# Optimization experiments

Measured on AMD Instinct MI355X. Metric: run time of the kernel, lower is better.

The kernel has to match this reference:

```python
import jax, jax.numpy as jnp
import numpy as np

B, L, S, DIM, H, DH, DFF = 2, 2048, 2048, 1024, 16, 64, 4096
EPS = 1e-6


def _ln(x, w, b):
    m = jnp.mean(x, axis=-1, keepdims=True)
    v = jnp.mean(jnp.square(x - m), axis=-1, keepdims=True)
    return (x - m) / jnp.sqrt(v + EPS) * w + b


def _mha(q, k, v, mask):
    # q: [B,L,H*DH], k/v: [B,S,H*DH], mask broadcastable to [B,H,L,S], True = masked
    b, l, _ = q.shape
    s = k.shape[1]
    q = q.reshape(b, l, H, DH)
    k = k.reshape(b, s, H, DH)
    v = v.reshape(b, s, H, DH)
    scale = 1.0 / np.sqrt(DH).astype(np.float32)
    attn = jnp.einsum('blhd,bshd->bhls', q, k) * scale
    if mask is not None:
        attn = jnp.where(mask, -jnp.inf, attn)
    attn = jax.nn.softmax(attn, axis=-1)
    out = jnp.einsum('bhls,bshd->blhd', attn, v)
    return out.reshape(b, l, H * DH)


def setup_inputs() -> dict:
    key = jax.random.key(0)
    ks = jax.random.split(key, 12)
    std = 0.02
    inp = {
        'input': jax.random.normal(ks[0], (B, L, DIM), jnp.float32),
        'source': jax.random.normal(ks[1], (B, S, DIM), jnp.float32),
        # source mask: no source positions masked
        'source_mask': jnp.zeros((B, 1, 1, S), bool),
        # causal mask for self-attention (True above diagonal -> masked)
        'mask': jnp.triu(jnp.ones((L, L), bool), 1)[None, None],
        # self-attention
        'ln_self_w': jnp.ones((DIM,), jnp.float32),
        'ln_self_b': jnp.zeros((DIM,), jnp.float32),
        'w_qkv': std * jax.random.normal(ks[2], (DIM, 3 * DIM), jnp.float32),
        'b_qkv': jnp.zeros((3 * DIM,), jnp.float32),
        'w_so': std * jax.random.normal(ks[3], (DIM, DIM), jnp.float32),
        'b_so': jnp.zeros((DIM,), jnp.float32),
        # cross-attention
        'ln_cross_w': jnp.ones((DIM,), jnp.float32),
        'ln_cross_b': jnp.zeros((DIM,), jnp.float32),
        'w_q': std * jax.random.normal(ks[4], (DIM, DIM), jnp.float32),
        'b_q': jnp.zeros((DIM,), jnp.float32),
        'w_kv': std * jax.random.normal(ks[5], (DIM, 2 * DIM), jnp.float32),
        'b_kv': jnp.zeros((2 * DIM,), jnp.float32),
        'w_co': std * jax.random.normal(ks[6], (DIM, DIM), jnp.float32),
        'b_co': jnp.zeros((DIM,), jnp.float32),
        # MLP (1 layer)
        'ln_mlp_w': jnp.ones((DIM,), jnp.float32),
        'ln_mlp_b': jnp.zeros((DIM,), jnp.float32),
        'w_ff1': std * jax.random.normal(ks[7], (DIM, DFF), jnp.float32),
        'b_ff1': jnp.zeros((DFF,), jnp.float32),
        'w_ff2': std * jax.random.normal(ks[8], (DFF, DIM), jnp.float32),
        'b_ff2': jnp.zeros((DIM,), jnp.float32),
    }
    return inp


def reference(input, source, source_mask, mask,
              ln_self_w, ln_self_b, w_qkv, b_qkv, w_so, b_so,
              ln_cross_w, ln_cross_b, w_q, b_q, w_kv, b_kv, w_co, b_co,
              ln_mlp_w, ln_mlp_b, w_ff1, b_ff1, w_ff2, b_ff2):
    x = input
    # self-attention block (pre-LN)
    h = _ln(x, ln_self_w, ln_self_b)
    qkv = h @ w_qkv + b_qkv
    q, k, v = jnp.split(qkv, 3, axis=-1)
    sa = _mha(q, k, v, mask) @ w_so + b_so
    x = x + sa
    # cross-attention block (pre-LN)
    h = _ln(x, ln_cross_w, ln_cross_b)
    q = h @ w_q + b_q
    kv = source @ w_kv + b_kv
    k, v = jnp.split(kv, 2, axis=-1)
    ca = _mha(q, k, v, source_mask) @ w_co + b_co
    x = x + ca
    # feed-forward block (pre-LN), eval mode (no dropout/droppath)
    h = _ln(x, ln_mlp_w, ln_mlp_b)
    ff = jax.nn.gelu(h @ w_ff1 + b_ff1, approximate=False) @ w_ff2 + b_ff2
    x = x + ff
    return x
```

## Files before the change

kernel.cpp:

```cpp
#include <hip/hip_runtime.h>
#include <hip/hip_bf16.h>
#include <math.h>

typedef __bf16 bf16_t;
typedef __bf16 bf16x8 __attribute__((ext_vector_type(8)));
typedef __bf16 bf16x4 __attribute__((ext_vector_type(4)));
typedef float  f32x4  __attribute__((ext_vector_type(4)));

#define DIM   1024
#define NB    2
#define NL    2048
#define NS    2048
#define NH    16
#define NDH   64
#define NDFF  4096

#define DS_READ_B128(dst, addr) \
    asm volatile("ds_read_b128 %0, %1" : "=v"(dst) : "v"(addr))
#define LGKM0_FENCE() do { \
    asm volatile("s_waitcnt lgkmcnt(0)" ::: "memory"); \
    __builtin_amdgcn_sched_barrier(0); } while (0)

__device__ __forceinline__ bf16x8 ld_bf16x8(const bf16_t* p) {
    return *reinterpret_cast<const bf16x8*>(p);
}

__device__ __forceinline__ void gl_lds16(const bf16_t* g, bf16_t* l) {
    __builtin_amdgcn_global_load_lds(
        (const __attribute__((address_space(1))) void*)g,
        (__attribute__((address_space(3))) void*)l, 16, 0, 0);
}

__device__ __forceinline__ unsigned lds_u32(const bf16_t* p) {
    return (unsigned)(uintptr_t)(__attribute__((address_space(3))) const void*)p;
}

__global__ __launch_bounds__(256)
void wconv_kernel(const float* __restrict__ in, bf16_t* __restrict__ out, int K, int N)
{
    __shared__ float tile[32][33];
    int n0 = blockIdx.x * 32, k0 = blockIdx.y * 32;
    int tx = threadIdx.x & 31, ty = threadIdx.x >> 5;
    #pragma unroll
    for (int j = 0; j < 4; ++j)
        tile[ty + 8*j][tx] = in[(size_t)(k0 + ty + 8*j) * N + n0 + tx];
    __syncthreads();
    #pragma unroll
    for (int j = 0; j < 4; ++j)
        out[(size_t)(n0 + ty + 8*j) * K + k0 + tx] = (bf16_t)tile[tx][ty + 8*j];
}

__global__ __launch_bounds__(256)
void f2b_kernel(const float* __restrict__ in, bf16_t* __restrict__ out)
{
    size_t i = ((size_t)blockIdx.x * 256 + threadIdx.x) * 4;
    float4 v = *reinterpret_cast<const float4*>(in + i);
    bf16x4 o = { (bf16_t)v.x, (bf16_t)v.y, (bf16_t)v.z, (bf16_t)v.w };
    *reinterpret_cast<bf16x4*>(out + i) = o;
}

__global__ __launch_bounds__(256)
void ln_kernel(const float* __restrict__ x, const float* __restrict__ wgt,
               const float* __restrict__ bia, bf16_t* __restrict__ out)
{
    int row = blockIdx.x, tid = threadIdx.x;
    float4 xv = reinterpret_cast<const float4*>(x + (size_t)row * DIM)[tid];
    float s1 = xv.x + xv.y + xv.z + xv.w;
    float s2 = xv.x*xv.x + xv.y*xv.y + xv.z*xv.z + xv.w*xv.w;
    #pragma unroll
    for (int off = 32; off > 0; off >>= 1) {
        s1 += __shfl_xor(s1, off, 64);
        s2 += __shfl_xor(s2, off, 64);
    }
    __shared__ float red[8];
    int w = tid >> 6;
    if ((tid & 63) == 0) { red[w] = s1; red[w + 4] = s2; }
    __syncthreads();
    s1 = red[0] + red[1] + red[2] + red[3];
    s2 = red[4] + red[5] + red[6] + red[7];
    float mean = s1 * (1.0f / DIM);
    float var  = s2 * (1.0f / DIM) - mean * mean;
    float rstd = rsqrtf(var + 1e-6f);
    float4 wv = reinterpret_cast<const float4*>(wgt)[tid];
    float4 bv = reinterpret_cast<const float4*>(bia)[tid];
    bf16x4 o = { (bf16_t)((xv.x - mean) * rstd * wv.x + bv.x),
                 (bf16_t)((xv.y - mean) * rstd * wv.y + bv.y),
                 (bf16_t)((xv.z - mean) * rstd * wv.z + bv.z),
                 (bf16_t)((xv.w - mean) * rstd * wv.w + bv.w) };
    reinterpret_cast<bf16x4*>(out + (size_t)row * DIM)[tid] = o;
}

template<int EPI, int BM, int BN>
__global__ __launch_bounds__(512)
void gemm_kernel(const bf16_t* __restrict__ A, const bf16_t* __restrict__ BT,
                 const float* __restrict__ bias, const float* __restrict__ res,
                 void* __restrict__ out, int M, int N, int K)
{
    constexpr int WM = BM / 2, WN = BN / 4;
    constexpr int AM = WM / 16, AN = WN / 16;
    constexpr int ABE = (BM + BN) * 64;
    __shared__ __align__(16) bf16_t lds[2 * ABE];

    int tid = threadIdx.x;
    int lane = tid & 63, w = tid >> 6;
    int wr = w >> 2, wc = w & 3;
    int la = lane & 15, lg = lane >> 4;

    int gx = gridDim.x;
    int flat = blockIdx.y * gx + blockIdx.x;
    int cpx = gx >> 3;
    int xcd = flat & 7, loc = flat >> 3;
    int m0 = (loc / cpx) * BM;
    int n0 = (xcd * cpx + loc % cpx) * BN;

    f32x4 acc[AM][AN] = {};

    int srl  = lane >> 3;
    int sch  = lane & 7;
    int scol = ((sch ^ srl) * 8);
    const bf16_t* Ap = A  + (size_t)(m0 + w * 8 + srl) * K + scol;
    const bf16_t* Bp = BT + (size_t)(n0 + w * 8 + srl) * K + scol;

    auto stage = [&](int t, int buf) {
        int k0 = t * 64;
        bf16_t* base = &lds[buf * ABE];
        #pragma unroll
        for (int i = 0; i < BM / 64; ++i)
            gl_lds16(Ap + ((size_t)i * 64) * K + k0, base + (i * 64 + w * 8) * 64);
        #pragma unroll
        for (int i = 0; i < BN / 64; ++i)
            gl_lds16(Bp + ((size_t)i * 64) * K + k0, base + (BM + i * 64 + w * 8) * 64);
    };

    unsigned ldsb = lds_u32(lds);
    unsigned kla = la & 7;
    unsigned a_base = ldsb + (wr * WM + la) * 128 + ((lg ^ kla) * 16);
    unsigned b_base = ldsb + BM * 128 + (wc * WN + la) * 128 + ((lg ^ kla) * 16);

    auto compute = [&](int buf) {
        unsigned dB = (unsigned)(buf * ABE * 2);
        bf16x8 af[AM], bfr[AN];
        #pragma unroll
        for (int mi = 0; mi < AM; ++mi)
            DS_READ_B128(af[mi], a_base + dB + mi * 2048);
        #pragma unroll
        for (int ni = 0; ni < AN; ++ni)
            DS_READ_B128(bfr[ni], b_base + dB + ni * 2048);
        LGKM0_FENCE();
        __builtin_amdgcn_s_setprio(1);
        #pragma unroll
        for (int mi = 0; mi < AM; ++mi)
            #pragma unroll
            for (int ni = 0; ni < AN; ++ni)
                acc[mi][ni] = __builtin_amdgcn_mfma_f32_16x16x32_bf16(
                                  af[mi], bfr[ni], acc[mi][ni], 0, 0, 0);
        __builtin_amdgcn_s_setprio(0);
        #pragma unroll
        for (int mi = 0; mi < AM; ++mi)
            DS_READ_B128(af[mi], (a_base + dB + mi * 2048) ^ 64u);
        #pragma unroll
        for (int ni = 0; ni < AN; ++ni)
            DS_READ_B128(bfr[ni], (b_base + dB + ni * 2048) ^ 64u);
        LGKM0_FENCE();
        __builtin_amdgcn_s_setprio(1);
        #pragma unroll
        for (int mi = 0; mi < AM; ++mi)
            #pragma unroll
            for (int ni = 0; ni < AN; ++ni)
                acc[mi][ni] = __builtin_amdgcn_mfma_f32_16x16x32_bf16(
                                  af[mi], bfr[ni], acc[mi][ni], 0, 0, 0);
        __builtin_amdgcn_s_setprio(0);
    };

    int nt = K / 64;
    stage(0, 0);
    for (int t = 0; t < nt; ++t) {
        asm volatile("s_waitcnt vmcnt(0)" ::: "memory");
        __builtin_amdgcn_s_barrier();
        __builtin_amdgcn_sched_barrier(0);
        if (t + 1 < nt) stage(t + 1, (t + 1) & 1);
        compute(t & 1);
    }

    #pragma unroll
    for (int mi = 0; mi < AM; ++mi) {
        #pragma unroll
        for (int ni = 0; ni < AN; ++ni) {
            #pragma unroll
            for (int i = 0; i < 4; ++i) {
                int row = m0 + wr * WM + mi * 16 + lg * 4 + i;
                int col = n0 + wc * WN + ni * 16 + la;
                float v = acc[mi][ni][i] + bias[col];
                if (EPI == 1) v = 0.5f * v * (1.0f + erff(v * 0.70710678118f));
                if (EPI == 2)
                    ((float*)out)[(size_t)row * N + col] = res[(size_t)row * N + col] + v;
                else
                    ((bf16_t*)out)[(size_t)row * N + col] = (bf16_t)v;
            }
        }
    }
}

template<bool CAUSAL>
__global__ __launch_bounds__(512)
void attn_kernel(const bf16_t* __restrict__ Q, int qs,
                 const bf16_t* __restrict__ Kp, int ks,
                 const bf16_t* __restrict__ Vp, int vs,
                 bf16_t* __restrict__ O, int os, int L, int S)
{
    __shared__ __align__(16) bf16_t Ks[64 * 64];
    __shared__ __align__(16) bf16_t Vt[64 * 64];
    __shared__ __align__(16) bf16_t Ps[8][16 * 64];

    int tid = threadIdx.x, lane = tid & 63, w = tid >> 6;
    int la = lane & 15, lg = lane >> 4;
    int qtile = (CAUSAL ? (gridDim.x - 1 - blockIdx.x) : blockIdx.x) * 128;
    int b = blockIdx.y >> 4, h = blockIdx.y & 15;

    const bf16_t* qb = Q  + (size_t)(b * L) * qs + h * 64;
    const bf16_t* kb = Kp + (size_t)(b * S) * ks + h * 64;
    const bf16_t* vb = Vp + (size_t)(b * S) * vs + h * 64;
    bf16_t*       ob = O  + (size_t)(b * L) * os + h * 64;

    int qrow = qtile + w * 16 + la;
    bf16x8 qf0 = ld_bf16x8(qb + (size_t)qrow * qs + lg * 8);
    bf16x8 qf1 = ld_bf16x8(qb + (size_t)qrow * qs + 32 + lg * 8);
    #pragma unroll
    for (int j = 0; j < 8; ++j) {
        qf0[j] = qf0[j] * (bf16_t)0.125f;
        qf1[j] = qf1[j] * (bf16_t)0.125f;
    }

    f32x4 zero = {0.f, 0.f, 0.f, 0.f};
    f32x4 o[4];
    #pragma unroll
    for (int dt = 0; dt < 4; ++dt) o[dt] = zero;
    float lpart[4] = {0.f, 0.f, 0.f, 0.f};

    int rk    = tid >> 3;
    int ck8   = tid & 7;
    int sv    = tid & 63;
    int dbase = (tid >> 6) * 8;
    int r7 = la & 7;

    int n_full = (CAUSAL ? qtile : S) / 64;
    int nit = n_full + (CAUSAL ? 2 : 0);

    bf16x8 kr = ld_bf16x8(kb + (size_t)rk * ks + ck8 * 8);
    bf16x8 vr = ld_bf16x8(vb + (size_t)sv * vs + dbase);

    for (int it = 0; it < nit; ++it) {
        int s0 = it * 64;
        bool diag = CAUSAL && (it >= n_full);

        __syncthreads();
        *reinterpret_cast<bf16x8*>(&Ks[rk * 64 + ((ck8 ^ (rk & 7)) * 8)]) = kr;
        #pragma unroll
        for (int j = 0; j < 8; ++j)
            Vt[(dbase + j) * 64 + (sv ^ (j << 3))] = vr[j];
        __syncthreads();

        if (it + 1 < nit) {
            int s1 = s0 + 64;
            kr = ld_bf16x8(kb + (size_t)(s1 + rk) * ks + ck8 * 8);
            vr = ld_bf16x8(vb + (size_t)(s1 + sv) * vs + dbase);
        }

        f32x4 sf[4];
        #pragma unroll
        for (int ct = 0; ct < 4; ++ct) {
            const bf16_t* kp = &Ks[(ct * 16 + la) * 64];
            bf16x8 k0 = ld_bf16x8(kp + ((lg ^ r7) * 8));
            bf16x8 k1 = ld_bf16x8(kp + (((4 + lg) ^ r7) * 8));
            f32x4 z = zero;
            __builtin_amdgcn_s_setprio(1);
            z = __builtin_amdgcn_mfma_f32_16x16x32_bf16(qf0, k0, z, 0, 0, 0);
            z = __builtin_amdgcn_mfma_f32_16x16x32_bf16(qf1, k1, z, 0, 0, 0);
            __builtin_amdgcn_s_setprio(0);
            sf[ct] = z;
        }

        #pragma unroll
        for (int ct = 0; ct < 4; ++ct) {
            #pragma unroll
            for (int i = 0; i < 4; ++i) {
                float p = __expf(sf[ct][i]);
                if (diag) {
                    int sg = s0 + ct * 16 + la;
                    int qg = qtile + w * 16 + lg * 4 + i;
                    if (sg > qg) p = 0.f;
                }
                lpart[i] += p;
                int row = lg * 4 + i;
                Ps[w][row * 64 + ((ct * 16 + la) ^ ((row & 7) << 3))] = (bf16_t)p;
            }
        }

        bf16x8 pa0 = ld_bf16x8(&Ps[w][la * 64 + ((lg ^ r7) * 8)]);
        bf16x8 pa1 = ld_bf16x8(&Ps[w][la * 64 + (((4 + lg) ^ r7) * 8)]);
        __builtin_amdgcn_s_setprio(1);
        #pragma unroll
        for (int dt = 0; dt < 4; ++dt) {
            const bf16_t* vp = &Vt[(dt * 16 + la) * 64];
            bf16x8 v0 = ld_bf16x8(vp + ((lg ^ r7) * 8));
            bf16x8 v1 = ld_bf16x8(vp + (((4 + lg) ^ r7) * 8));
            o[dt] = __builtin_amdgcn_mfma_f32_16x16x32_bf16(pa0, v0, o[dt], 0, 0, 0);
            o[dt] = __builtin_amdgcn_mfma_f32_16x16x32_bf16(pa1, v1, o[dt], 0, 0, 0);
        }
        __builtin_amdgcn_s_setprio(0);
    }

    #pragma unroll
    for (int off = 1; off < 16; off <<= 1)
        #pragma unroll
        for (int i = 0; i < 4; ++i)
            lpart[i] += __shfl_xor(lpart[i], off, 64);

    #pragma unroll
    for (int dt = 0; dt < 4; ++dt)
        #pragma unroll
        for (int i = 0; i < 4; ++i) {
            int row = qtile + w * 16 + lg * 4 + i;
            float val = o[dt][i] / lpart[i];
            ob[(size_t)row * os + dt * 16 + la] = (bf16_t)val;
        }
}

extern "C" void kernel_launch(void* const* d_in, const int* in_sizes, int n_in,
                              void* d_out, int out_size, void* d_ws, size_t ws_size,
                              hipStream_t stream)
{
    const float* input     = (const float*)d_in[0];
    const float* source    = (const float*)d_in[1];
    const float* ln_self_w = (const float*)d_in[4];
    const float* ln_self_b = (const float*)d_in[5];
    const float* w_qkv     = (const float*)d_in[6];
    const float* b_qkv     = (const float*)d_in[7];
    const float* w_so      = (const float*)d_in[8];
    const float* b_so      = (const float*)d_in[9];
    const float* ln_cross_w= (const float*)d_in[10];
    const float* ln_cross_b= (const float*)d_in[11];
    const float* w_q       = (const float*)d_in[12];
    const float* b_q       = (const float*)d_in[13];
    const float* w_kv      = (const float*)d_in[14];
    const float* b_kv      = (const float*)d_in[15];
    const float* w_co      = (const float*)d_in[16];
    const float* b_co      = (const float*)d_in[17];
    const float* ln_mlp_w  = (const float*)d_in[18];
    const float* ln_mlp_b  = (const float*)d_in[19];
    const float* w_ff1     = (const float*)d_in[20];
    const float* b_ff1     = (const float*)d_in[21];
    const float* w_ff2     = (const float*)d_in[22];
    const float* b_ff2     = (const float*)d_in[23];

    const int M = NB * NL;

    char* ws = (char*)d_ws;
    size_t off = 0;
    auto alloc = [&](size_t bytes) { char* p = ws + off; off += (bytes + 255) & ~(size_t)255; return p; };

    bf16_t* wT_qkv = (bf16_t*)alloc((size_t)3072 * 1024 * 2);
    bf16_t* wT_so  = (bf16_t*)alloc((size_t)1024 * 1024 * 2);
    bf16_t* wT_q   = (bf16_t*)alloc((size_t)1024 * 1024 * 2);
    bf16_t* wT_kv  = (bf16_t*)alloc((size_t)2048 * 1024 * 2);
    bf16_t* wT_co  = (bf16_t*)alloc((size_t)1024 * 1024 * 2);
    bf16_t* wT_ff1 = (bf16_t*)alloc((size_t)4096 * 1024 * 2);
    bf16_t* wT_ff2 = (bf16_t*)alloc((size_t)1024 * 4096 * 2);
    bf16_t* srcb   = (bf16_t*)alloc((size_t)M * 1024 * 2);
    bf16_t* hbuf   = (bf16_t*)alloc((size_t)M * 1024 * 2);
    bf16_t* qkvb   = (bf16_t*)alloc((size_t)M * 3072 * 2);
    bf16_t* attnb  = (bf16_t*)alloc((size_t)M * 1024 * 2);
    bf16_t* qcb    = (bf16_t*)alloc((size_t)M * 1024 * 2);
    bf16_t* kvcb   = (bf16_t*)alloc((size_t)M * 2048 * 2);
    float*  xbuf   = (float*) alloc((size_t)M * 1024 * 4);
    bf16_t* ff1b   = (bf16_t*)alloc((size_t)M * 4096 * 2);
    (void)ws_size; (void)n_in; (void)in_sizes; (void)out_size;

    wconv_kernel<<<dim3(3072/32, 1024/32), 256, 0, stream>>>(w_qkv, wT_qkv, 1024, 3072);
    wconv_kernel<<<dim3(1024/32, 1024/32), 256, 0, stream>>>(w_so,  wT_so,  1024, 1024);
    wconv_kernel<<<dim3(1024/32, 1024/32), 256, 0, stream>>>(w_q,   wT_q,   1024, 1024);
    wconv_kernel<<<dim3(2048/32, 1024/32), 256, 0, stream>>>(w_kv,  wT_kv,  1024, 2048);
    wconv_kernel<<<dim3(1024/32, 1024/32), 256, 0, stream>>>(w_co,  wT_co,  1024, 1024);
    wconv_kernel<<<dim3(4096/32, 1024/32), 256, 0, stream>>>(w_ff1, wT_ff1, 1024, 4096);
    wconv_kernel<<<dim3(1024/32, 4096/32), 256, 0, stream>>>(w_ff2, wT_ff2, 4096, 1024);
    f2b_kernel<<<(M * 1024) / (256 * 4), 256, 0, stream>>>(source, srcb);

    ln_kernel<<<M, 256, 0, stream>>>(input, ln_self_w, ln_self_b, hbuf);
    gemm_kernel<0,128,128><<<dim3(3072/128, M/128), 512, 0, stream>>>(hbuf, wT_qkv, b_qkv, nullptr, qkvb, M, 3072, 1024);
    attn_kernel<true><<<dim3(NL/128, NB*NH), 512, 0, stream>>>(qkvb, 3072, qkvb + 1024, 3072, qkvb + 2048, 3072,
                                                               attnb, 1024, NL, NL);
    gemm_kernel<2,128,64><<<dim3(1024/64, M/128), 512, 0, stream>>>(attnb, wT_so, b_so, input, xbuf, M, 1024, 1024);

    ln_kernel<<<M, 256, 0, stream>>>(xbuf, ln_cross_w, ln_cross_b, hbuf);
    gemm_kernel<0,128,64><<<dim3(1024/64, M/128), 512, 0, stream>>>(hbuf, wT_q, b_q, nullptr, qcb, M, 1024, 1024);
    gemm_kernel<0,128,128><<<dim3(2048/128, M/128), 512, 0, stream>>>(srcb, wT_kv, b_kv, nullptr, kvcb, M, 2048, 1024);
    attn_kernel<false><<<dim3(NL/128, NB*NH), 512, 0, stream>>>(qcb, 1024, kvcb, 2048, kvcb + 1024, 2048,
                                                                attnb, 1024, NL, NS);
    gemm_kernel<2,128,64><<<dim3(1024/64, M/128), 512, 0, stream>>>(attnb, wT_co, b_co, xbuf, xbuf, M, 1024, 1024);

    ln_kernel<<<M, 256, 0, stream>>>(xbuf, ln_mlp_w, ln_mlp_b, hbuf);
    gemm_kernel<1,128,128><<<dim3(4096/128, M/128), 512, 0, stream>>>(hbuf, wT_ff1, b_ff1, nullptr, ff1b, M, 4096, 1024);
    gemm_kernel<2,128,64><<<dim3(1024/64, M/128), 512, 0, stream>>>(ff1b, wT_ff2, b_ff2, xbuf, d_out, M, 1024, 4096);
}
```

Measured before the change: 387.5 us.

## Split attention KV range across two blocks and combine partial outputs

Both attention launches gain a third grid dimension of two splits, each covering half of the key/value tiles. Each split writes unnormalized fp32 output and row sums to scratch buffers that reuse ff1b, qcb and hbuf. A new elementwise kernel adds the two partials, divides by the combined sum and writes bf16. The goal is to double the number of blocks and even out causal work across CUs. The cost is an extra launch plus a large fp32 round trip through global memory per attention.

```diff
diff --git a/kernel.cpp b/kernel.cpp
--- a/kernel.cpp
+++ b/kernel.cpp
@@ -206,7 +206,8 @@
 void attn_kernel(const bf16_t* __restrict__ Q, int qs,
                  const bf16_t* __restrict__ Kp, int ks,
                  const bf16_t* __restrict__ Vp, int vs,
-                 bf16_t* __restrict__ O, int os, int L, int S)
+                 float* __restrict__ o_part, float* __restrict__ l_part,
+                 int L, int S)
 {
     __shared__ __align__(16) bf16_t Ks[64 * 64];
     __shared__ __align__(16) bf16_t Vt[64 * 64];
@@ -216,11 +217,11 @@
     int la = lane & 15, lg = lane >> 4;
     int qtile = (CAUSAL ? (gridDim.x - 1 - blockIdx.x) : blockIdx.x) * 128;
     int b = blockIdx.y >> 4, h = blockIdx.y & 15;
+    int split = blockIdx.z;
 
     const bf16_t* qb = Q  + (size_t)(b * L) * qs + h * 64;
     const bf16_t* kb = Kp + (size_t)(b * S) * ks + h * 64;
     const bf16_t* vb = Vp + (size_t)(b * S) * vs + h * 64;
-    bf16_t*       ob = O  + (size_t)(b * L) * os + h * 64;
 
     int qrow = qtile + w * 16 + la;
     bf16x8 qf0 = ld_bf16x8(qb + (size_t)qrow * qs + lg * 8);
@@ -244,12 +245,15 @@
     int r7 = la & 7;
 
     int n_full = (CAUSAL ? qtile : S) / 64;
-    int nit = n_full + (CAUSAL ? 2 : 0);
-
-    bf16x8 kr = ld_bf16x8(kb + (size_t)rk * ks + ck8 * 8);
-    bf16x8 vr = ld_bf16x8(vb + (size_t)sv * vs + dbase);
-
-    for (int it = 0; it < nit; ++it) {
+    int ntot = CAUSAL ? (n_full + 2) : (S / 64);
+    int mid = ntot >> 1;
+    int lo = split ? mid : 0;
+    int hi = split ? ntot : mid;
+
+    bf16x8 kr = ld_bf16x8(kb + (size_t)(lo * 64 + rk) * ks + ck8 * 8);
+    bf16x8 vr = ld_bf16x8(vb + (size_t)(lo * 64 + sv) * vs + dbase);
+
+    for (int it = lo; it < hi; ++it) {
         int s0 = it * 64;
         bool diag = CAUSAL && (it >= n_full);
 
@@ -260,7 +264,7 @@
             Vt[(dbase + j) * 64 + (sv ^ (j << 3))] = vr[j];
         __syncthreads();
 
-        if (it + 1 < nit) {
+        if (it + 1 < hi) {
             int s1 = s0 + 64;
             kr = ld_bf16x8(kb + (size_t)(s1 + rk) * ks + ck8 * 8);
             vr = ld_bf16x8(vb + (size_t)(s1 + sv) * vs + dbase);
@@ -317,13 +321,31 @@
             lpart[i] += __shfl_xor(lpart[i], off, 64);
 
     #pragma unroll
-    for (int dt = 0; dt < 4; ++dt)
-        #pragma unroll
-        for (int i = 0; i < 4; ++i) {
-            int row = qtile + w * 16 + lg * 4 + i;
-            float val = o[dt][i] / lpart[i];
-            ob[(size_t)row * os + dt * 16 + la] = (bf16_t)val;
-        }
+    for (int i = 0; i < 4; ++i) {
+        size_t rowg = (size_t)(b * L + qtile + w * 16 + lg * 4 + i);
+        #pragma unroll
+        for (int dt = 0; dt < 4; ++dt)
+            o_part[((size_t)split * 4096 + rowg) * 1024 + h * 64 + dt * 16 + la] = o[dt][i];
+        if (la == 0)
+            l_part[((size_t)split * 4096 + rowg) * 16 + h] = lpart[i];
+    }
+}
+
+__global__ __launch_bounds__(256)
+void attn_comb_kernel(const float* __restrict__ op, const float* __restrict__ lp,
+                      bf16_t* __restrict__ out)
+{
+    size_t i = ((size_t)blockIdx.x * 256 + threadIdx.x) * 4;
+    const size_t OS = (size_t)4096 * 1024;
+    float4 a = *reinterpret_cast<const float4*>(op + i);
+    float4 c = *reinterpret_cast<const float4*>(op + OS + i);
+    size_t row = i >> 10;
+    int h = (int)((i & 1023) >> 6);
+    float l = lp[row * 16 + h] + lp[(4096 + row) * 16 + h];
+    float rl = 1.0f / l;
+    bf16x4 o = { (bf16_t)((a.x + c.x) * rl), (bf16_t)((a.y + c.y) * rl),
+                 (bf16_t)((a.z + c.z) * rl), (bf16_t)((a.w + c.w) * rl) };
+    *reinterpret_cast<bf16x4*>(out + i) = o;
 }
 
 extern "C" void kernel_launch(void* const* d_in, const int* in_sizes, int n_in,
@@ -376,6 +398,8 @@
     bf16_t* ff1b   = (bf16_t*)alloc((size_t)M * 4096 * 2);
     (void)ws_size; (void)n_in; (void)in_sizes; (void)out_size;
 
+    float* o_part = (float*)ff1b;
+
     wconv_kernel<<<dim3(3072/32, 1024/32), 256, 0, stream>>>(w_qkv, wT_qkv, 1024, 3072);
     wconv_kernel<<<dim3(1024/32, 1024/32), 256, 0, stream>>>(w_so,  wT_so,  1024, 1024);
     wconv_kernel<<<dim3(1024/32, 1024/32), 256, 0, stream>>>(w_q,   wT_q,   1024, 1024);
@@ -387,15 +411,17 @@
 
     ln_kernel<<<M, 256, 0, stream>>>(input, ln_self_w, ln_self_b, hbuf);
     gemm_kernel<0,128,128><<<dim3(3072/128, M/128), 512, 0, stream>>>(hbuf, wT_qkv, b_qkv, nullptr, qkvb, M, 3072, 1024);
-    attn_kernel<true><<<dim3(NL/128, NB*NH), 512, 0, stream>>>(qkvb, 3072, qkvb + 1024, 3072, qkvb + 2048, 3072,
-                                                               attnb, 1024, NL, NL);
+    attn_kernel<true><<<dim3(NL/128, NB*NH, 2), 512, 0, stream>>>(qkvb, 3072, qkvb + 1024, 3072, qkvb + 2048, 3072,
+                                                                  o_part, (float*)qcb, NL, NL);
+    attn_comb_kernel<<<(M * 1024) / (256 * 4), 256, 0, stream>>>(o_part, (float*)qcb, attnb);
     gemm_kernel<2,128,64><<<dim3(1024/64, M/128), 512, 0, stream>>>(attnb, wT_so, b_so, input, xbuf, M, 1024, 1024);
 
     ln_kernel<<<M, 256, 0, stream>>>(xbuf, ln_cross_w, ln_cross_b, hbuf);
     gemm_kernel<0,128,64><<<dim3(1024/64, M/128), 512, 0, stream>>>(hbuf, wT_q, b_q, nullptr, qcb, M, 1024, 1024);
     gemm_kernel<0,128,128><<<dim3(2048/128, M/128), 512, 0, stream>>>(srcb, wT_kv, b_kv, nullptr, kvcb, M, 2048, 1024);
-    attn_kernel<false><<<dim3(NL/128, NB*NH), 512, 0, stream>>>(qcb, 1024, kvcb, 2048, kvcb + 1024, 2048,
-                                                                attnb, 1024, NL, NS);
+    attn_kernel<false><<<dim3(NL/128, NB*NH, 2), 512, 0, stream>>>(qcb, 1024, kvcb, 2048, kvcb + 1024, 2048,
+                                                                   o_part, (float*)hbuf, NL, NS);
+    attn_comb_kernel<<<(M * 1024) / (256 * 4), 256, 0, stream>>>(o_part, (float*)hbuf, attnb);
     gemm_kernel<2,128,64><<<dim3(1024/64, M/128), 512, 0, stream>>>(attnb, wT_co, b_co, xbuf, xbuf, M, 1024, 1024);
 
     ln_kernel<<<M, 256, 0, stream>>>(xbuf, ln_mlp_w, ln_mlp_b, hbuf);
```

After: 401.8 us. 1.04x slower.
